# Optimization experiments

Measured on AMD Instinct MI355X. Metric: run time of the kernel, lower is better.

Reference implementation:

```python
import jax, jax.numpy as jnp
import numpy as np

FEATS = 512   # F, forced by groups=512
K = 8         # kernel_size arg (number of shifted taps)
L = 3         # lag
CK = 3        # actual Conv1d kernel width
OUT_CH = K * FEATS * L  # 12288


def setup_inputs() -> dict:
    key = jax.random.key(0)
    k1, k2, k3 = jax.random.split(key, 3)
    M, T = 4, 1024
    x = jax.random.normal(k1, (M, T, FEATS), dtype=jnp.float32)
    # grouped conv: out_channels=12288, in_channels/groups = 512/512 = 1, width 3
    conv_w = jax.random.normal(k2, (OUT_CH, 1, CK), dtype=jnp.float32) * 0.1
    conv_b = jax.random.normal(k3, (OUT_CH,), dtype=jnp.float32) * 0.1
    return {"x": x, "conv_w": conv_w, "conv_b": conv_b}


def reference(x, conv_w, conv_b):
    M, T, F = x.shape
    # causal grouped conv: left-pad CK-1, feature_group_count = F
    xc = jnp.transpose(x, (0, 2, 1))  # (M, F, T)
    y = jax.lax.conv_general_dilated(
        xc, conv_w, window_strides=(1,), padding=[(CK - 1, 0)],
        dimension_numbers=("NCH", "OIH", "NCH"), feature_group_count=F)
    y = y + conv_b[None, :, None]                   # (M, OUT_CH, T)
    y = jnp.transpose(y, (0, 2, 1)).reshape(M, T, F, K, L)

    t = jnp.arange(T)
    lag_slices = []
    for l in range(L):
        taps = []
        for i in range(K):
            s = i + l
            # NOTE: original torch code rolls along the FEATURE axis (dim 2 of (M,T,F))
            z = jnp.roll(y[:, :, :, i, l], s, axis=2)      # (M, T, F)
            # ... but zeros the first s TIME steps (faithful reproduction)
            z = jnp.where((t >= s)[None, :, None], z, 0.0)
            taps.append(z)
        lag_slices.append(jnp.stack(taps, axis=-1))        # (M, T, F, K)
    x_new = jnp.stack(lag_slices, axis=0)                   # (L, M, T, F, K)
    x_new = x_new.reshape(L * M, T, F, K)
    return jnp.transpose(x_new, (2, 1, 0, 3))               # (F, T, L*M, K)
```

## Files before the change

kernel.cpp:

```cpp
#include <hip/hip_runtime.h>


typedef float f32x4 __attribute__((ext_vector_type(4)));

#define NF 512
#define NT 1024
#define FB 16
#define TT 32
#define XROW 25
#define NROWS (TT + 2)
#define XM (NROWS * XROW)
#define SLAB (4 * XM)

__global__ __launch_bounds__(384, 4) void caconv_kernel(
    const float* __restrict__ x,
    const float* __restrict__ w,
    const float* __restrict__ b,
    float* __restrict__ out)
{
    __shared__ float x_lds[SLAB];
    __shared__ float w_lds[FB * 72];
    __shared__ float b_lds[FB * 24];

    const int tid = threadIdx.x;
    const int f0  = (blockIdx.x >> 5) * FB;
    const int t0  = (blockIdx.x & 31) * TT;

    for (int i = tid; i < FB * 96; i += 384) {
        if (i < FB * 72) {
            const int fl = i / 72, r = i - fl * 72;
            const int l = r / 24, r2 = r - l * 24, tap = r2 >> 3, k = r2 & 7;
            const int fs = (f0 + fl - k - l + NF) & (NF - 1);
            w_lds[i] = w[(fs * 24 + k * 3 + l) * 3 + tap];
        } else {
            const int j = i - FB * 72;
            const int fl = j / 24, r = j - fl * 24, l = r >> 3, k = r & 7;
            const int fs = (f0 + fl - k - l + NF) & (NF - 1);
            b_lds[j] = b[fs * 24 + k * 3 + l];
        }
    }

    for (int i = tid; i < SLAB; i += 384) {
        const int fi  = i % XROW;
        const int row = i / XROW;
        const int tt  = row % NROWS;
        const int m   = row / NROWS;
        const int tg  = t0 - 2 + tt;
        const int fs  = (f0 - 9 + fi + NF) & (NF - 1);
        float v = 0.0f;
        if (tg >= 0) v = x[((m << 10) + tg) * NF + fs];
        x_lds[m * XM + tt * XROW + fi] = v;
    }
    __syncthreads();

    const int fl = tid / 24;
    const int u  = tid - fl * 24;
    const int lm = u >> 1;
    const int k0 = (u & 1) << 2;
    const int l  = lm >> 2;
    const int m  = lm & 3;
    const int fib = fl + 6 - l - k0;

    const float* wp = w_lds + fl * 72 + l * 24 + k0;
    const f32x4 w0 = *(const f32x4*)(wp);
    const f32x4 w1 = *(const f32x4*)(wp + 8);
    const f32x4 w2 = *(const f32x4*)(wp + 16);
    const f32x4 bias = *(const f32x4*)(b_lds + fl * 24 + l * 8 + k0);

    const float* xp = x_lds + m * XM + fib;
    float* outp = out + ((size_t)(f0 + fl) * NT + t0) * 96 + lm * 8 + k0;

    f32x4 rA, rB, rC;
    rA[0] = xp[0];  rA[1] = xp[1];  rA[2] = xp[2];  rA[3] = xp[3];
    rB[0] = xp[XROW]; rB[1] = xp[XROW+1]; rB[2] = xp[XROW+2]; rB[3] = xp[XROW+3];

#pragma unroll 4
    for (int t_off = 0; t_off < TT; ++t_off) {
        const float* rp = xp + (t_off + 2) * XROW;
        rC[0] = rp[0]; rC[1] = rp[1]; rC[2] = rp[2]; rC[3] = rp[3];

        f32x4 acc = bias;
        acc[0] += w0[0] * rA[3]; acc[1] += w0[1] * rA[2];
        acc[2] += w0[2] * rA[1]; acc[3] += w0[3] * rA[0];
        acc[0] += w1[0] * rB[3]; acc[1] += w1[1] * rB[2];
        acc[2] += w1[2] * rB[1]; acc[3] += w1[3] * rB[0];
        acc[0] += w2[0] * rC[3]; acc[1] += w2[1] * rC[2];
        acc[2] += w2[2] * rC[1]; acc[3] += w2[3] * rC[0];

        if (t0 == 0 && t_off < 10) {
#pragma unroll
            for (int kk = 0; kk < 4; ++kk)
                if (t_off < k0 + kk + l) acc[kk] = 0.0f;
        }

        *(f32x4*)outp = acc;
        outp += 96;

        rA = rB; rB = rC;
    }
}

extern "C" void kernel_launch(void* const* d_in, const int* in_sizes, int n_in,
                              void* d_out, int out_size, void* d_ws, size_t ws_size,
                              hipStream_t stream)
{
    const float* x = (const float*)d_in[0];
    const float* w = (const float*)d_in[1];
    const float* b = (const float*)d_in[2];
    float* out = (float*)d_out;

    const int grid = (NF / FB) * (NT / TT);
    caconv_kernel<<<grid, 384, 0, stream>>>(x, w, b, out);
}
```

Baseline: 39.63 us.

## Process two time tiles per block with register-prefetched double-buffered input

Each block now covers two consecutive 32-step time tiles, which halves the grid and amortizes the weight/bias staging across both tiles. The second tile's input slab is loaded into registers while the first tile is computed, then written to a second LDS buffer after a sync. Address math is precomputed once and reused for both loads. The cost is fewer blocks, a lower occupancy hint (3 instead of 4), more LDS and more registers per thread.

```diff
diff --git a/kernel.cpp b/kernel.cpp
--- a/kernel.cpp
+++ b/kernel.cpp
@@ -11,20 +11,23 @@
 #define NROWS (TT + 2)
 #define XM (NROWS * XROW)
 #define SLAB (4 * XM)
+#define SLABA (SLAB + 8)
+#define NIT 9
+#define DUMMY SLAB
 
-__global__ __launch_bounds__(384, 4) void caconv_kernel(
+__global__ __launch_bounds__(384, 3) void caconv_kernel(
     const float* __restrict__ x,
     const float* __restrict__ w,
     const float* __restrict__ b,
     float* __restrict__ out)
 {
-    __shared__ float x_lds[SLAB];
+    __shared__ float x_lds[2 * SLABA];
     __shared__ float w_lds[FB * 72];
     __shared__ float b_lds[FB * 24];
 
-    const int tid = threadIdx.x;
-    const int f0  = (blockIdx.x >> 5) * FB;
-    const int t0  = (blockIdx.x & 31) * TT;
+    const int tid   = threadIdx.x;
+    const int f0    = (blockIdx.x >> 4) * FB;
+    const int tbase = (blockIdx.x & 15) * (2 * TT);
 
     for (int i = tid; i < FB * 96; i += 384) {
         if (i < FB * 72) {
@@ -40,17 +43,35 @@
         }
     }
 
-    for (int i = tid; i < SLAB; i += 384) {
-        const int fi  = i % XROW;
-        const int row = i / XROW;
-        const int tt  = row % NROWS;
-        const int m   = row / NROWS;
-        const int tg  = t0 - 2 + tt;
-        const int fs  = (f0 - 9 + fi + NF) & (NF - 1);
+    int goff[NIT], pk[NIT];
+#pragma unroll
+    for (int it = 0; it < NIT; ++it) {
+        const int i = tid + it * 384;
+        if (i < SLAB) {
+            const int fi  = i % XROW;
+            const int row = i / XROW;
+            const int tt  = row % NROWS;
+            const int m   = row / NROWS;
+            const int fs  = (f0 - 9 + fi + NF) & (NF - 1);
+            goff[it] = ((tt - 2) << 9) + fs;
+            pk[it]   = ((m * XM + tt * XROW + fi) << 2) | m;
+        } else {
+            goff[it] = -(1 << 30);
+            pk[it]   = DUMMY << 2;
+        }
+    }
+
+    float r[NIT];
+
+#pragma unroll
+    for (int it = 0; it < NIT; ++it) {
+        const int g = goff[it] + (tbase << 9);
         float v = 0.0f;
-        if (tg >= 0) v = x[((m << 10) + tg) * NF + fs];
-        x_lds[m * XM + tt * XROW + fi] = v;
+        if (g >= 0) v = x[g + ((pk[it] & 3) << 19)];
+        r[it] = v;
     }
+#pragma unroll
+    for (int it = 0; it < NIT; ++it) x_lds[pk[it] >> 2] = r[it];
     __syncthreads();
 
     const int fl = tid / 24;
@@ -67,36 +88,58 @@
     const f32x4 w2 = *(const f32x4*)(wp + 16);
     const f32x4 bias = *(const f32x4*)(b_lds + fl * 24 + l * 8 + k0);
 
-    const float* xp = x_lds + m * XM + fib;
-    float* outp = out + ((size_t)(f0 + fl) * NT + t0) * 96 + lm * 8 + k0;
+#pragma unroll 1
+    for (int j = 0; j < 2; ++j) {
+        const int t0 = tbase + j * TT;
 
-    f32x4 rA, rB, rC;
-    rA[0] = xp[0];  rA[1] = xp[1];  rA[2] = xp[2];  rA[3] = xp[3];
-    rB[0] = xp[XROW]; rB[1] = xp[XROW+1]; rB[2] = xp[XROW+2]; rB[3] = xp[XROW+3];
+        if (j == 0) {
+            const int t1s = (tbase + TT) << 9;
+#pragma unroll
+            for (int it = 0; it < NIT; ++it) {
+                const int g = goff[it] + t1s;
+                float v = 0.0f;
+                if (g >= 0) v = x[g + ((pk[it] & 3) << 19)];
+                r[it] = v;
+            }
+        }
+
+        const float* xp = x_lds + j * SLABA + m * XM + fib;
+        float* outp = out + ((size_t)(f0 + fl) * NT + t0) * 96 + lm * 8 + k0;
+
+        f32x4 rA, rB, rC;
+        rA[0] = xp[0];  rA[1] = xp[1];  rA[2] = xp[2];  rA[3] = xp[3];
+        rB[0] = xp[XROW]; rB[1] = xp[XROW+1]; rB[2] = xp[XROW+2]; rB[3] = xp[XROW+3];
 
 #pragma unroll 4
-    for (int t_off = 0; t_off < TT; ++t_off) {
-        const float* rp = xp + (t_off + 2) * XROW;
-        rC[0] = rp[0]; rC[1] = rp[1]; rC[2] = rp[2]; rC[3] = rp[3];
+        for (int t_off = 0; t_off < TT; ++t_off) {
+            const float* rp = xp + (t_off + 2) * XROW;
+            rC[0] = rp[0]; rC[1] = rp[1]; rC[2] = rp[2]; rC[3] = rp[3];
 
-        f32x4 acc = bias;
-        acc[0] += w0[0] * rA[3]; acc[1] += w0[1] * rA[2];
-        acc[2] += w0[2] * rA[1]; acc[3] += w0[3] * rA[0];
-        acc[0] += w1[0] * rB[3]; acc[1] += w1[1] * rB[2];
-        acc[2] += w1[2] * rB[1]; acc[3] += w1[3] * rB[0];
-        acc[0] += w2[0] * rC[3]; acc[1] += w2[1] * rC[2];
-        acc[2] += w2[2] * rC[1]; acc[3] += w2[3] * rC[0];
+            f32x4 acc = bias;
+            acc[0] += w0[0] * rA[3]; acc[1] += w0[1] * rA[2];
+            acc[2] += w0[2] * rA[1]; acc[3] += w0[3] * rA[0];
+            acc[0] += w1[0] * rB[3]; acc[1] += w1[1] * rB[2];
+            acc[2] += w1[2] * rB[1]; acc[3] += w1[3] * rB[0];
+            acc[0] += w2[0] * rC[3]; acc[1] += w2[1] * rC[2];
+            acc[2] += w2[2] * rC[1]; acc[3] += w2[3] * rC[0];
 
-        if (t0 == 0 && t_off < 10) {
+            if (t0 == 0 && t_off < 10) {
 #pragma unroll
-            for (int kk = 0; kk < 4; ++kk)
-                if (t_off < k0 + kk + l) acc[kk] = 0.0f;
+                for (int kk = 0; kk < 4; ++kk)
+                    if (t_off < k0 + kk + l) acc[kk] = 0.0f;
+            }
+
+            *(f32x4*)outp = acc;
+            outp += 96;
+
+            rA = rB; rB = rC;
         }
 
-        *(f32x4*)outp = acc;
-        outp += 96;
-
-        rA = rB; rB = rC;
+        if (j == 0) {
+#pragma unroll
+            for (int it = 0; it < NIT; ++it) x_lds[SLABA + (pk[it] >> 2)] = r[it];
+            __syncthreads();
+        }
     }
 }
 
@@ -109,6 +152,6 @@
     const float* b = (const float*)d_in[2];
     float* out = (float*)d_out;
 
-    const int grid = (NF / FB) * (NT / TT);
+    const int grid = (NF / FB) * (NT / (2 * TT));
     caconv_kernel<<<grid, 384, 0, stream>>>(x, w, b, out);
 }
```

Measured after the change: 38.57 us. 2.7% less time.
